# Kernel optimization log

Hardware: AMD Instinct MI355X
Metric: run time of the kernel (lower is better)

Reference implementation:

```python
import jax, jax.numpy as jnp
from jax import lax
import numpy as np

# torch.sign(torch.sign(x) + 0.5): maps x<0 -> -1, x>=0 -> +1 (zeros go to +1)
def binarize(x):
    return jnp.where(x >= 0, 1.0, -1.0).astype(x.dtype)


def setup_inputs() -> dict:
    key = jax.random.key(0)
    kx, kw, kb = jax.random.split(key, 3)
    x = jax.random.normal(kx, (32, 256, 56, 56), dtype=jnp.float32)
    weight = jax.random.normal(kw, (256, 256, 3, 3), dtype=jnp.float32)
    bias = jax.random.normal(kb, (256,), dtype=jnp.float32)
    return {"x": x, "weight": weight, "bias": bias}


def reference(x, weight, bias):
    b_weight = binarize(weight)  # [O, I, kH, kW] in {-1, +1}
    b_bias = binarize(bias)      # [O] in {-1, +1}
    out = lax.conv_general_dilated(
        x, b_weight,
        window_strides=(1, 1),
        padding=((1, 1), (1, 1)),
        rhs_dilation=(1, 1),
        feature_group_count=1,
        dimension_numbers=("NCHW", "OIHW", "NCHW"),
    )
    return out + b_bias[None, :, None, None]
```

## Files before the change

kernel.cpp:

```cpp
#include <hip/hip_runtime.h>
#include <stdint.h>


#define N_IMG 32
#define C_IN  256
#define H_IN  56
#define W_IN  56
#define O_OUT 256
#define HW    (H_IN * W_IN)
#define K_RAW (C_IN * 9)

typedef int8_t i8x16 __attribute__((ext_vector_type(16)));
typedef int    i32x4 __attribute__((ext_vector_type(4)));
typedef float  f32x4 __attribute__((ext_vector_type(4)));
typedef float  f32x4u __attribute__((ext_vector_type(4), aligned(4)));
typedef __bf16 bf16x8 __attribute__((ext_vector_type(8)));

#define WQ_BYTES ((size_t)36 * 256 * 64)
#define AM_OFF   WQ_BYTES
#define WS_NEED  (AM_OFF + 64)

#define BPITCH  80
#define BS_ROWB (58 * BPITCH)
#define CHUNK_B (3 * 8192)

#define AMAX_BLOCKS 1024

#define AS1 __attribute__((address_space(1)))
#define AS3 __attribute__((address_space(3)))

__device__ __forceinline__ void dma16(const void* g, void* l) {
    __builtin_amdgcn_global_load_lds((const AS1 uint32_t*)g, (AS3 uint32_t*)l, 16, 0, 0);
}

__global__ void prep_combo(const float* __restrict__ x, const float* __restrict__ w,
                           int8_t* __restrict__ wq, unsigned* __restrict__ am_bits) {
    __shared__ __attribute__((aligned(16))) int8_t S[9 * 64 * 64];
    const int bx = blockIdx.x;
    const int t  = threadIdx.x;

    if (bx >= 16) {
        const int b = bx - 16;
        const size_t NV = (size_t)N_IMG * C_IN * HW / 4;
        float m = 0.f;
        for (size_t i = (size_t)b * 256 + t; i < NV; i += (size_t)AMAX_BLOCKS * 256) {
            f32x4 v = ((const f32x4*)x)[i];
            m = fmaxf(m, fmaxf(fmaxf(fabsf(v[0]), fabsf(v[1])),
                               fmaxf(fabsf(v[2]), fabsf(v[3]))));
        }
#pragma unroll
        for (int off = 32; off; off >>= 1)
            m = fmaxf(m, __shfl_down(m, off));
        float* red = (float*)S;
        if ((t & 63) == 0) red[t >> 6] = m;
        __syncthreads();
        if (t == 0) {
            m = fmaxf(fmaxf(red[0], red[1]), fmaxf(red[2], red[3]));
            atomicMax(am_bits, __float_as_uint(m));
        }
        return;
    }

    const int og = bx >> 2;
    const int cc = bx & 3;
    const int o0 = og * 64;
#pragma unroll
    for (int kk = 0; kk < 4; ++kk) {
        const int p   = kk * 256 + t;
        const int o_l = p >> 4;
        const int chg = p & 15;
        const float* src = w + (size_t)(o0 + o_l) * K_RAW + (size_t)(cc * 64 + chg * 4) * 9;
        f32x4u v[9];
#pragma unroll
        for (int q = 0; q < 9; ++q) v[q] = *(const f32x4u*)(src + q * 4);
#pragma unroll
        for (int tap = 0; tap < 9; ++tap) {
            unsigned dw = 0;
#pragma unroll
            for (int co = 0; co < 4; ++co) {
                const int flat = co * 9 + tap;
                const float fv = v[flat >> 2][flat & 3];
                dw |= (unsigned)((fv >= 0.f) ? 0x01u : 0xffu) << (co * 8);
            }
            *(unsigned*)&S[tap * 4096 + o_l * 64 + chg * 4] = dw;
        }
    }
    __syncthreads();
#pragma unroll
    for (int kk = 0; kk < 9; ++kk) {
        const int c    = kk * 256 + t;
        const int tap  = c >> 8;
        const int rem  = c & 255;
        const int o_l  = rem >> 2;
        const int cpos = rem & 3;
        const int truec = (cpos - ((o_l & 15) >> 1)) & 3;
        i32x4 vv = *(const i32x4*)&S[tap * 4096 + o_l * 64 + truec * 16];
        *(i32x4*)(wq + ((size_t)(cc * 9 + tap) * 256 + (o0 + o_l)) * 64 + cpos * 16) = vv;
    }
}

__launch_bounds__(256, 2)
__global__ void bconv_fx(const float* __restrict__ x,
                         const int8_t* __restrict__ wq,
                         const float* __restrict__ bias,
                         const unsigned* __restrict__ amax_bits,
                         float* __restrict__ out) {
    __shared__ __attribute__((aligned(16))) int8_t As[2 * CHUNK_B];
    __shared__ __attribute__((aligned(16))) int8_t Bs[6 * BS_ROWB];

    const int tid  = threadIdx.x;
    const int lane = tid & 63;
    const int wv   = tid >> 6;
    const int row  = lane & 15;
    const int quad = lane >> 4;

    const int nrp  = blockIdx.x;
    const int n    = nrp / 14;
    const int rp   = nrp - n * 14;
    const int oblk = blockIdx.y;
    const int h0   = rp * 4;

    const float am    = __uint_as_float(*amax_bits);
    const float scale = 127.f / fmaxf(am, 1e-20f);
    const float inv   = am * (1.0f / 127.0f);

    int pr[4], pc[4];
    bool live[4];
#pragma unroll
    for (int nt = 0; nt < 4; ++nt) {
        int p = wv * 64 + nt * 16 + row;
        live[nt] = (p < 224);
        int r = p / 56;
        int c = p - r * 56;
        if (!live[nt]) { r = 0; c = 0; }
        pr[nt] = r;
        pc[nt] = c;
    }

    i32x4 acc[8][4];
#pragma unroll
    for (int mt = 0; mt < 8; ++mt)
#pragma unroll
        for (int nt = 0; nt < 4; ++nt)
            acc[mt][nt] = (i32x4){0, 0, 0, 0};

    const int rowA = row * 64 + (((quad + (row >> 1)) & 3) << 4);
    int addrB[4];
#pragma unroll
    for (int nt = 0; nt < 4; ++nt)
        addrB[nt] = pr[nt] * BS_ROWB + pc[nt] * BPITCH + quad * 16;

    auto issueA3 = [&](int c) {
        const int8_t* g = wq + (size_t)(3 * c) * 16384 + oblk * 8192 + wv * 2048 + lane * 16;
        int8_t* l = &As[(c & 1) * CHUNK_B + wv * 2048];
#pragma unroll
        for (int u = 0; u < 3; ++u) {
            dma16(g + u * 16384,        l + u * 8192);
            dma16(g + u * 16384 + 1024, l + u * 8192 + 1024);
        }
    };

    issueA3(0);

    const int wg = tid & 15;
    const int cg = tid >> 4;

    i32x4 af[8], bc[4], bn[4];

    for (int cc = 0; cc < 4; ++cc) {
        __syncthreads();

        {
            const float* xpl = x + ((size_t)n * C_IN + cc * 64 + cg * 4) * HW;
#pragma unroll 2
            for (int r6 = 0; r6 < 6; ++r6) {
                const int hin = h0 + r6 - 1;
                int8_t* lrow = &Bs[r6 * BS_ROWB];
                if (wg >= 14) {
                    const int ww = (wg == 14) ? 0 : 57;
                    *(int*)(lrow + ww * BPITCH + cg * 4) = 0;
                } else if ((unsigned)hin < 56u) {
                    const float* src = xpl + (size_t)hin * W_IN + wg * 4;
                    f32x4 v0 = *(const f32x4*)(src);
                    f32x4 v1 = *(const f32x4*)(src + HW);
                    f32x4 v2 = *(const f32x4*)(src + 2 * HW);
                    f32x4 v3 = *(const f32x4*)(src + 3 * HW);
#pragma unroll
                    for (int k = 0; k < 4; ++k) {
                        float f0 = fminf(fmaxf(v0[k] * scale, -127.f), 127.f);
                        float f1 = fminf(fmaxf(v1[k] * scale, -127.f), 127.f);
                        float f2 = fminf(fmaxf(v2[k] * scale, -127.f), 127.f);
                        float f3 = fminf(fmaxf(v3[k] * scale, -127.f), 127.f);
                        int d = ((int)(uint8_t)(int8_t)(int)rintf(f0))
                              | ((int)(uint8_t)(int8_t)(int)rintf(f1) << 8)
                              | ((int)(uint8_t)(int8_t)(int)rintf(f2) << 16)
                              | ((int)(uint8_t)(int8_t)(int)rintf(f3) << 24);
                        *(int*)(lrow + (wg * 4 + k + 1) * BPITCH + cg * 4) = d;
                    }
                } else {
#pragma unroll
                    for (int k = 0; k < 4; ++k)
                        *(int*)(lrow + (wg * 4 + k + 1) * BPITCH + cg * 4) = 0;
                }
            }
        }
        __syncthreads();

#pragma unroll
        for (int k = 0; k < 3; ++k) {
            const int c = cc * 3 + k;
            if (k == 0) {
                if (c + 1 < 12) issueA3(c + 1);
#pragma unroll
                for (int nt = 0; nt < 4; ++nt)
                    bc[nt] = *(const i32x4*)(&Bs[addrB[nt]]);
            } else {
                __syncthreads();
                if (c + 1 < 12) issueA3(c + 1);
#pragma unroll
                for (int nt = 0; nt < 4; ++nt) bc[nt] = bn[nt];
            }
            const int8_t* Acur = &As[(c & 1) * CHUNK_B];
#pragma unroll
            for (int mt = 0; mt < 8; ++mt)
                af[mt] = *(const i32x4*)(Acur + mt * 1024 + rowA);

#pragma unroll
            for (int u = 0; u < 3; ++u) {
                if (u < 2) {
                    const int offn = k * BS_ROWB + (u + 1) * BPITCH;
#pragma unroll
                    for (int nt = 0; nt < 4; ++nt)
                        bn[nt] = *(const i32x4*)(&Bs[addrB[nt] + offn]);
                    const int8_t* Anx = Acur + (u + 1) * 8192;
#pragma unroll
                    for (int mt = 0; mt < 8; ++mt) {
                        i32x4 a = af[mt];
#pragma unroll
                        for (int nt = 0; nt < 4; ++nt)
                            acc[mt][nt] = __builtin_amdgcn_mfma_i32_16x16x64_i8(
                                a, bc[nt], acc[mt][nt], 0, 0, 0);
                        af[mt] = *(const i32x4*)(Anx + mt * 1024 + rowA);
                    }
#pragma unroll
                    for (int nt = 0; nt < 4; ++nt) bc[nt] = bn[nt];
                } else {
                    if (k < 2) {
                        const int offn = (k + 1) * BS_ROWB;
#pragma unroll
                        for (int nt = 0; nt < 4; ++nt)
                            bn[nt] = *(const i32x4*)(&Bs[addrB[nt] + offn]);
                    }
#pragma unroll
                    for (int mt = 0; mt < 8; ++mt)
#pragma unroll
                        for (int nt = 0; nt < 4; ++nt)
                            acc[mt][nt] = __builtin_amdgcn_mfma_i32_16x16x64_i8(
                                af[mt], bc[nt], acc[mt][nt], 0, 0, 0);
                }
            }
        }
    }

    float* base0 = out + ((size_t)n * O_OUT + oblk * 128) * HW;
    int pixoff[4];
#pragma unroll
    for (int nt = 0; nt < 4; ++nt)
        pixoff[nt] = (h0 + pr[nt]) * W_IN + pc[nt];
#pragma unroll
    for (int mt = 0; mt < 8; ++mt) {
        f32x4 bv = *(const f32x4*)(bias + oblk * 128 + mt * 16 + quad * 4);
#pragma unroll
        for (int r = 0; r < 4; ++r) {
            const float sb = (bv[r] >= 0.0f) ? 1.0f : -1.0f;
            const size_t ob = (size_t)(mt * 16 + quad * 4 + r) * HW;
#pragma unroll
            for (int nt = 0; nt < 4; ++nt)
                if (live[nt]) base0[ob + pixoff[nt]] = (float)acc[mt][nt][r] * inv + sb;
        }
    }
}

#define CHW (C_IN * HW)
#define FPITCH 40

__launch_bounds__(256, 2)
__global__ void bconv_fallback(const float* __restrict__ x,
                               const float* __restrict__ w,
                               const float* __restrict__ bias,
                               float* __restrict__ out) {
    __shared__ __attribute__((aligned(16))) __bf16 Asf[128 * FPITCH];
    __shared__ __attribute__((aligned(16))) __bf16 Bsf[128 * FPITCH];

    const int tid  = threadIdx.x;
    const int lane = tid & 63;
    const int wv   = tid >> 6;
    const int pblk = blockIdx.x;
    const int oblk = blockIdx.y;

    const int p_local = tid & 127;
    const int cgrp    = tid >> 7;
    const int pixel   = pblk * 128 + p_local;
    const int n_img   = pixel / HW;
    const int hw      = pixel - n_img * HW;
    const int h       = hw / W_IN;
    const int wx      = hw - h * W_IN;
    const float* xbase = x + (size_t)n_img * CHW;

    f32x4 acc[8][2];
#pragma unroll
    for (int mt = 0; mt < 8; ++mt)
#pragma unroll
        for (int nt = 0; nt < 2; ++nt)
            acc[mt][nt] = (f32x4){0.f, 0.f, 0.f, 0.f};

    const int pix_wave = wv * 32;
    const int row  = lane & 15;
    const int quad = lane >> 4;

    for (int tap = 0; tap < 9; ++tap) {
        const int dh = tap / 3 - 1;
        const int dw = tap % 3 - 1;
        const int hh = h + dh;
        const int ww = wx + dw;
        const bool valid = ((unsigned)hh < (unsigned)H_IN) && ((unsigned)ww < (unsigned)W_IN);
        const int offs = hh * W_IN + ww;

        for (int ck = 0; ck < 8; ++ck) {
            __syncthreads();
#pragma unroll
            for (int rep = 0; rep < 2; ++rep) {
                int v  = tid + rep * 256;
                int oa = v >> 2;
                int c8 = v & 3;
                const float* wsrc = w + (size_t)(oblk * 128 + oa) * K_RAW
                                      + (ck * 32 + c8 * 8) * 9 + tap;
                bf16x8 val;
#pragma unroll
                for (int j = 0; j < 8; ++j)
                    val[j] = (wsrc[j * 9] >= 0.0f) ? (__bf16)1.0f : (__bf16)(-1.0f);
                *(bf16x8*)(&Asf[oa * FPITCH + c8 * 8]) = val;
            }
            {
                const int cbase = (ck * 32 + cgrp * 16) * HW + offs;
#pragma unroll
                for (int g = 0; g < 2; ++g) {
                    bf16x8 vb;
#pragma unroll
                    for (int j = 0; j < 8; ++j) {
                        float f = valid ? xbase[cbase + (g * 8 + j) * HW] : 0.0f;
                        vb[j] = (__bf16)f;
                    }
                    *(bf16x8*)(&Bsf[p_local * FPITCH + cgrp * 16 + g * 8]) = vb;
                }
            }
            __syncthreads();
            bf16x8 bfrag[2];
#pragma unroll
            for (int nt = 0; nt < 2; ++nt)
                bfrag[nt] = *(const bf16x8*)(&Bsf[(pix_wave + nt * 16 + row) * FPITCH + quad * 8]);
#pragma unroll
            for (int mt = 0; mt < 8; ++mt) {
                bf16x8 afrag = *(const bf16x8*)(&Asf[(mt * 16 + row) * FPITCH + quad * 8]);
#pragma unroll
                for (int nt = 0; nt < 2; ++nt)
                    acc[mt][nt] = __builtin_amdgcn_mfma_f32_16x16x32_bf16(
                        afrag, bfrag[nt], acc[mt][nt], 0, 0, 0);
            }
        }
    }

#pragma unroll
    for (int nt = 0; nt < 2; ++nt) {
        int pix = pblk * 128 + pix_wave + nt * 16 + row;
        int ni  = pix / HW;
        int phw = pix - ni * HW;
        float* obase = out + (size_t)ni * (O_OUT * HW) + phw;
#pragma unroll
        for (int mt = 0; mt < 8; ++mt) {
            int o0 = oblk * 128 + mt * 16 + quad * 4;
#pragma unroll
            for (int r = 0; r < 4; ++r) {
                int o = o0 + r;
                float sb = (bias[o] >= 0.0f) ? 1.0f : -1.0f;
                obase[(size_t)o * HW] = acc[mt][nt][r] + sb;
            }
        }
    }
}

extern "C" void kernel_launch(void* const* d_in, const int* in_sizes, int n_in,
                              void* d_out, int out_size, void* d_ws, size_t ws_size,
                              hipStream_t stream) {
    const float* x    = (const float*)d_in[0];
    const float* w    = (const float*)d_in[1];
    const float* bias = (const float*)d_in[2];
    float* out        = (float*)d_out;

    if (ws_size >= WS_NEED) {
        int8_t*   wq = (int8_t*)d_ws;
        unsigned* am = (unsigned*)((char*)d_ws + AM_OFF);

        hipMemsetAsync(am, 0, 4, stream);
        prep_combo<<<dim3(16 + AMAX_BLOCKS), dim3(256), 0, stream>>>(x, w, wq, am);
        bconv_fx<<<dim3(N_IMG * 14, 2), dim3(256), 0, stream>>>(x, wq, bias, am, out);
    } else {
        bconv_fallback<<<dim3((N_IMG * HW) / 128, 2), dim3(256), 0, stream>>>(
            x, w, bias, out);
    }
}
```

Measured before the change: 276.8 us.

## Fuse per-tile activation absmax into conv kernel, drop global amax pass

Removes the separate whole-tensor absmax reduction over x, along with its memset and atomic. Each conv block now computes the max over its own input tile and reduces it through shared memory, so the quantization scale becomes per-tile instead of global. The tile is read once for the max and again during quantization, and that second read should mostly hit cache. The 4 LDS stores per thread are also rotated by lane group to reduce bank conflicts. This trades a full extra pass over the ~100MB input for redundant per-block reads, and it changes quantization numerics slightly.

```diff
diff --git a/kernel.cpp b/kernel.cpp
--- a/kernel.cpp
+++ b/kernel.cpp
@@ -17,15 +17,12 @@
 typedef __bf16 bf16x8 __attribute__((ext_vector_type(8)));
 
 #define WQ_BYTES ((size_t)36 * 256 * 64)
-#define AM_OFF   WQ_BYTES
-#define WS_NEED  (AM_OFF + 64)
+#define WS_NEED  WQ_BYTES
 
 #define BPITCH  80
 #define BS_ROWB (58 * BPITCH)
 #define CHUNK_B (3 * 8192)
 
-#define AMAX_BLOCKS 1024
-
 #define AS1 __attribute__((address_space(1)))
 #define AS3 __attribute__((address_space(3)))
 
@@ -33,34 +30,10 @@
     __builtin_amdgcn_global_load_lds((const AS1 uint32_t*)g, (AS3 uint32_t*)l, 16, 0, 0);
 }
 
-__global__ void prep_combo(const float* __restrict__ x, const float* __restrict__ w,
-                           int8_t* __restrict__ wq, unsigned* __restrict__ am_bits) {
+__global__ void prep_w(const float* __restrict__ w, int8_t* __restrict__ wq) {
     __shared__ __attribute__((aligned(16))) int8_t S[9 * 64 * 64];
     const int bx = blockIdx.x;
     const int t  = threadIdx.x;
-
-    if (bx >= 16) {
-        const int b = bx - 16;
-        const size_t NV = (size_t)N_IMG * C_IN * HW / 4;
-        float m = 0.f;
-        for (size_t i = (size_t)b * 256 + t; i < NV; i += (size_t)AMAX_BLOCKS * 256) {
-            f32x4 v = ((const f32x4*)x)[i];
-            m = fmaxf(m, fmaxf(fmaxf(fabsf(v[0]), fabsf(v[1])),
-                               fmaxf(fabsf(v[2]), fabsf(v[3]))));
-        }
-#pragma unroll
-        for (int off = 32; off; off >>= 1)
-            m = fmaxf(m, __shfl_down(m, off));
-        float* red = (float*)S;
-        if ((t & 63) == 0) red[t >> 6] = m;
-        __syncthreads();
-        if (t == 0) {
-            m = fmaxf(fmaxf(red[0], red[1]), fmaxf(red[2], red[3]));
-            atomicMax(am_bits, __float_as_uint(m));
-        }
-        return;
-    }
-
     const int og = bx >> 2;
     const int cc = bx & 3;
     const int o0 = og * 64;
@@ -100,13 +73,13 @@
 }
 
 __launch_bounds__(256, 2)
-__global__ void bconv_fx(const float* __restrict__ x,
-                         const int8_t* __restrict__ wq,
-                         const float* __restrict__ bias,
-                         const unsigned* __restrict__ amax_bits,
-                         float* __restrict__ out) {
+__global__ void bconv_fx2(const float* __restrict__ x,
+                          const int8_t* __restrict__ wq,
+                          const float* __restrict__ bias,
+                          float* __restrict__ out) {
     __shared__ __attribute__((aligned(16))) int8_t As[2 * CHUNK_B];
     __shared__ __attribute__((aligned(16))) int8_t Bs[6 * BS_ROWB];
+    __shared__ float sred[4];
 
     const int tid  = threadIdx.x;
     const int lane = tid & 63;
@@ -120,9 +93,49 @@
     const int oblk = blockIdx.y;
     const int h0   = rp * 4;
 
-    const float am    = __uint_as_float(*amax_bits);
-    const float scale = 127.f / fmaxf(am, 1e-20f);
-    const float inv   = am * (1.0f / 127.0f);
+    const int wg = tid & 15;
+    const int cg = tid >> 4;
+
+    auto issueA3 = [&](int c) {
+        const int8_t* g = wq + (size_t)(3 * c) * 16384 + oblk * 8192 + wv * 2048 + lane * 16;
+        int8_t* l = &As[(c & 1) * CHUNK_B + wv * 2048];
+#pragma unroll
+        for (int u = 0; u < 3; ++u) {
+            dma16(g + u * 16384,        l + u * 8192);
+            dma16(g + u * 16384 + 1024, l + u * 8192 + 1024);
+        }
+    };
+    issueA3(0);
+
+    float m = 0.f;
+    if (wg < 14) {
+        const float* xb = x + ((size_t)n * C_IN + cg * 4) * HW + wg * 4;
+#pragma unroll
+        for (int cc = 0; cc < 4; ++cc) {
+            const float* xpl = xb + (size_t)cc * 64 * HW;
+#pragma unroll 2
+            for (int r6 = 0; r6 < 6; ++r6) {
+                const int hin = h0 + r6 - 1;
+                if ((unsigned)hin < 56u) {
+                    const float* src = xpl + (size_t)hin * W_IN;
+#pragma unroll
+                    for (int j = 0; j < 4; ++j) {
+                        f32x4 v = *(const f32x4*)(src + (size_t)j * HW);
+                        m = fmaxf(m, fmaxf(fmaxf(fabsf(v[0]), fabsf(v[1])),
+                                           fmaxf(fabsf(v[2]), fabsf(v[3]))));
+                    }
+                }
+            }
+        }
+    }
+#pragma unroll
+    for (int off = 32; off; off >>= 1)
+        m = fmaxf(m, __shfl_down(m, off));
+    if (lane == 0) sred[wv] = m;
+    __syncthreads();
+    m = fmaxf(fmaxf(sred[0], sred[1]), fmaxf(sred[2], sred[3]));
+    const float scale = 127.f / fmaxf(m, 1e-20f);
+    const float inv   = m * (1.0f / 127.0f);
 
     int pr[4], pc[4];
     bool live[4];
@@ -149,21 +162,6 @@
 #pragma unroll
     for (int nt = 0; nt < 4; ++nt)
         addrB[nt] = pr[nt] * BS_ROWB + pc[nt] * BPITCH + quad * 16;
-
-    auto issueA3 = [&](int c) {
-        const int8_t* g = wq + (size_t)(3 * c) * 16384 + oblk * 8192 + wv * 2048 + lane * 16;
-        int8_t* l = &As[(c & 1) * CHUNK_B + wv * 2048];
-#pragma unroll
-        for (int u = 0; u < 3; ++u) {
-            dma16(g + u * 16384,        l + u * 8192);
-            dma16(g + u * 16384 + 1024, l + u * 8192 + 1024);
-        }
-    };
-
-    issueA3(0);
-
-    const int wg = tid & 15;
-    const int cg = tid >> 4;
 
     i32x4 af[8], bc[4], bn[4];
 
@@ -185,22 +183,29 @@
                     f32x4 v1 = *(const f32x4*)(src + HW);
                     f32x4 v2 = *(const f32x4*)(src + 2 * HW);
                     f32x4 v3 = *(const f32x4*)(src + 3 * HW);
+                    int d[4];
 #pragma unroll
                     for (int k = 0; k < 4; ++k) {
                         float f0 = fminf(fmaxf(v0[k] * scale, -127.f), 127.f);
                         float f1 = fminf(fmaxf(v1[k] * scale, -127.f), 127.f);
                         float f2 = fminf(fmaxf(v2[k] * scale, -127.f), 127.f);
                         float f3 = fminf(fmaxf(v3[k] * scale, -127.f), 127.f);
-                        int d = ((int)(uint8_t)(int8_t)(int)rintf(f0))
-                              | ((int)(uint8_t)(int8_t)(int)rintf(f1) << 8)
-                              | ((int)(uint8_t)(int8_t)(int)rintf(f2) << 16)
-                              | ((int)(uint8_t)(int8_t)(int)rintf(f3) << 24);
-                        *(int*)(lrow + (wg * 4 + k + 1) * BPITCH + cg * 4) = d;
+                        d[k] = ((int)(uint8_t)(int8_t)(int)rintf(f0))
+                             | ((int)(uint8_t)(int8_t)(int)rintf(f1) << 8)
+                             | ((int)(uint8_t)(int8_t)(int)rintf(f2) << 16)
+                             | ((int)(uint8_t)(int8_t)(int)rintf(f3) << 24);
+                    }
+#pragma unroll
+                    for (int kk = 0; kk < 4; ++kk) {
+                        const int k = (kk + wg) & 3;
+                        *(int*)(lrow + (wg * 4 + k + 1) * BPITCH + cg * 4) = d[k];
                     }
                 } else {
 #pragma unroll
-                    for (int k = 0; k < 4; ++k)
+                    for (int kk = 0; kk < 4; ++kk) {
+                        const int k = (kk + wg) & 3;
                         *(int*)(lrow + (wg * 4 + k + 1) * BPITCH + cg * 4) = 0;
+                    }
                 }
             }
         }
@@ -398,12 +403,9 @@
     float* out        = (float*)d_out;
 
     if (ws_size >= WS_NEED) {
-        int8_t*   wq = (int8_t*)d_ws;
-        unsigned* am = (unsigned*)((char*)d_ws + AM_OFF);
-
-        hipMemsetAsync(am, 0, 4, stream);
-        prep_combo<<<dim3(16 + AMAX_BLOCKS), dim3(256), 0, stream>>>(x, w, wq, am);
-        bconv_fx<<<dim3(N_IMG * 14, 2), dim3(256), 0, stream>>>(x, wq, bias, am, out);
+        int8_t* wq = (int8_t*)d_ws;
+        prep_w<<<dim3(16), dim3(256), 0, stream>>>(w, wq);
+        bconv_fx2<<<dim3(N_IMG * 14, 2), dim3(256), 0, stream>>>(x, wq, bias, out);
     } else {
         bconv_fallback<<<dim3((N_IMG * HW) / 128, 2), dim3(256), 0, stream>>>(
             x, w, bias, out);
```

Result: slower. 297.8 us (+7.6%).
